# Kernel optimization log

Measured on AMD Instinct MI355X. Metric: run time of the kernel, lower is better.

Reference implementation:

```python
import jax, jax.numpy as jnp
import numpy as np


def setup_inputs() -> dict:
    key = jax.random.key(0)
    k1, k2, k3, k4 = jax.random.split(key, 4)
    B, S, D_IN, D_OUT = 4, 4096, 768, 128
    x = jax.random.normal(k1, (B, S, D_IN), dtype=jnp.float32)
    # torch Linear(d_in, d_out) weight is [d_out, d_in]; we store transposed [d_in, d_out]
    scale = 1.0 / np.sqrt(D_IN)
    Wq = jax.random.normal(k2, (D_IN, D_OUT), dtype=jnp.float32) * scale
    Wk = jax.random.normal(k3, (D_IN, D_OUT), dtype=jnp.float32) * scale
    Wv = jax.random.normal(k4, (D_IN, D_OUT), dtype=jnp.float32) * scale
    return {"x": x, "Wq": Wq, "Wk": Wk, "Wv": Wv}


def reference(x, Wq, Wk, Wv):
    # x: [B, S, d_in]; Wq/Wk/Wv: [d_in, d_out]
    B, S, _ = x.shape
    q = jnp.einsum('bsd,de->bse', x, Wq)
    k = jnp.einsum('bsd,de->bse', x, Wk)
    v = jnp.einsum('bsd,de->bse', x, Wv)
    d_out = k.shape[-1]
    scores = jnp.einsum('bqe,bke->bqk', q, k)  # [B, S, S]
    causal = jnp.tril(jnp.ones((S, S), dtype=bool))  # True where attention allowed
    scores = jnp.where(causal[None], scores, -jnp.inf)
    attn = jax.nn.softmax(scores / jnp.sqrt(jnp.float32(d_out)), axis=-1)
    # dropout prob is 0.0 -> identity
    return jnp.einsum('bqk,bke->bqe', attn, v)
```

## Files before the change

### kernel.cpp

```cpp
#include <hip/hip_runtime.h>
#include <stdint.h>

typedef unsigned short u16;
typedef uint32_t u32;
typedef __bf16 bf16;
typedef bf16 bf16x8 __attribute__((ext_vector_type(8)));
typedef bf16 bf16x4 __attribute__((ext_vector_type(4)));
typedef short s16x4 __attribute__((ext_vector_type(4)));
typedef float f32x4 __attribute__((ext_vector_type(4)));
typedef uint32_t u32x4 __attribute__((ext_vector_type(4)));

#define S_LEN 4096
#define D_IN 768
#define D_OUT 128
#define NB 4
#define M_TOTAL (NB * S_LEN)
#define NPROP 115

__device__ const unsigned char SPLITS_T[16] = {1,2,3,4,4,5,6,7,8,8,9,10,11,12,12,13};
__device__ const unsigned char OFF_T[16]    = {0,1,3,6,10,14,19,25,32,40,48,57,67,78,90,102};
__device__ const unsigned char TILE_OF[NPROP] = {
    0, 1,1, 2,2,2, 3,3,3,3, 4,4,4,4, 5,5,5,5,5, 6,6,6,6,6,6, 7,7,7,7,7,7,7,
    8,8,8,8,8,8,8,8, 9,9,9,9,9,9,9,9, 10,10,10,10,10,10,10,10,10,
    11,11,11,11,11,11,11,11,11,11, 12,12,12,12,12,12,12,12,12,12,12,
    13,13,13,13,13,13,13,13,13,13,13,13, 14,14,14,14,14,14,14,14,14,14,14,14,
    15,15,15,15,15,15,15,15,15,15,15,15,15};

static __device__ __forceinline__ u16 f2bf(float f) {
    union { float f; uint32_t u; } c; c.f = f;
    return (u16)((c.u + 0x7FFFu + ((c.u >> 16) & 1u)) >> 16);
}
static __device__ __forceinline__ float bf2f_lo(uint32_t w) { return __uint_as_float(w << 16); }
static __device__ __forceinline__ float bf2f_hi(uint32_t w) { return __uint_as_float(w & 0xFFFF0000u); }

static __device__ __forceinline__ bf16x8 ld8(const u16* p) {
    union { u32x4 v; bf16x8 b; } c;
    c.v = *reinterpret_cast<const u32x4*>(p);
    return c.b;
}

static __device__ __forceinline__ f32x4 mfma16(bf16x8 a, bf16x8 b, f32x4 c) {
    return __builtin_amdgcn_mfma_f32_16x16x32_bf16(a, b, c, 0, 0, 0);
}

static __device__ __forceinline__ f32x4 mfma16k16(uint2 a, uint2 b, f32x4 c) {
#if defined(__HIP_DEVICE_COMPILE__)
#if __has_builtin(__builtin_amdgcn_mfma_f32_16x16x16_bf16)
    union { uint2 u; bf16x4 v; } ca, cb; ca.u = a; cb.u = b;
    return __builtin_amdgcn_mfma_f32_16x16x16_bf16(ca.v, cb.v, c, 0, 0, 0);
#else
    union { uint2 u; s16x4 v; } ca, cb; ca.u = a; cb.u = b;
    return __builtin_amdgcn_mfma_f32_16x16x16bf16_1k(ca.v, cb.v, c, 0, 0, 0);
#endif
#else
    (void)a; (void)b;
    return c;
#endif
}

static __device__ __forceinline__ void gload16(const void* g, void* l) {
    __builtin_amdgcn_global_load_lds((const __attribute__((address_space(1))) uint32_t*)g,
                                     (__attribute__((address_space(3))) uint32_t*)l, 16, 0, 0);
}

static __device__ __forceinline__ float bpermf(int addr, float v) {
    return __int_as_float(__builtin_amdgcn_ds_bpermute(addr, __float_as_int(v)));
}
static __device__ __forceinline__ u32 pk2(float a, float b) {
    return __builtin_amdgcn_perm(__float_as_uint(b), __float_as_uint(a), 0x07060302u);
}

__global__ __launch_bounds__(256) void wt_kernel(const float* __restrict__ Wq, const float* __restrict__ Wk,
                                                 const float* __restrict__ Wv, u16* __restrict__ Wt) {
    __shared__ u16 tl[128][40];
    const int w = blockIdx.x / 24;
    const int kc = (blockIdx.x % 24) * 32;
    const float* W = (w == 0) ? Wq : (w == 1) ? Wk : Wv;
#pragma unroll
    for (int p = 0; p < 4; ++p) {
        int kr = p * 8 + (threadIdx.x >> 5);
        int nc = (threadIdx.x & 31) * 4;
        float4 v = *reinterpret_cast<const float4*>(W + (size_t)(kc + kr) * D_OUT + nc);
        tl[nc + 0][kr] = f2bf(v.x); tl[nc + 1][kr] = f2bf(v.y);
        tl[nc + 2][kr] = f2bf(v.z); tl[nc + 3][kr] = f2bf(v.w);
    }
    __syncthreads();
    const int n = threadIdx.x >> 1, kh = (threadIdx.x & 1) * 16;
    u32x4* dst = reinterpret_cast<u32x4*>(Wt + (size_t)w * D_OUT * D_IN + (size_t)n * D_IN + kc + kh);
    const u32x4* src = reinterpret_cast<const u32x4*>(&tl[n][kh]);
    dst[0] = src[0];
    dst[1] = src[1];
}

__global__ __launch_bounds__(256) void qkv_kernel(const float* __restrict__ x, const u16* __restrict__ Wt,
                                                  u16* __restrict__ Qb, u16* __restrict__ Kb,
                                                  u16* __restrict__ Vt) {
    __shared__ __align__(16) u16 wslab[2][192 * 32];
    __shared__ __align__(16) float xslab[2][64 * 32];
    const int wave = threadIdx.x >> 6, lane = threadIdx.x & 63;
    const int r = lane & 15, g = lane >> 4;
    const int m0 = blockIdx.x * 64;
    const int h = blockIdx.y;

    f32x4 acc[3][4];
#pragma unroll
    for (int y = 0; y < 3; ++y)
#pragma unroll
        for (int f = 0; f < 4; ++f) acc[y][f] = f32x4{0.f, 0.f, 0.f, 0.f};

    auto stageW = [&](int bb, int kk) {
#pragma unroll
        for (int i = 0; i < 3; ++i) {
            int c = i * 4 + wave;
            int rr = c * 16 + (lane >> 2);
            int gr = (rr >> 6) * 128 + h * 64 + (rr & 63);
            const u16* src = Wt + (size_t)gr * D_IN + kk * 32 + (((lane & 3) ^ (rr & 3)) * 8);
            gload16(src, &wslab[bb][c * 512]);
        }
    };
    auto stageX = [&](int bb, int kk) {
#pragma unroll
        for (int i = 0; i < 2; ++i) {
            int c = i * 4 + wave;
            int row = c * 8 + (lane >> 3);
            const float* src = x + (size_t)(m0 + row) * D_IN + kk * 32 + (((lane & 7) ^ (row & 7)) * 4);
            gload16(src, &xslab[bb][c * 256]);
        }
    };

    stageW(0, 0);
    stageX(0, 0);
    int buf = 0;
    const int arow = wave * 16 + r;
    for (int kk = 0; kk < 24; ++kk) {
        int kn = (kk + 1 < 24) ? kk + 1 : 0;
        stageX(buf ^ 1, kn);
        stageW(buf ^ 1, kn);
        asm volatile("s_waitcnt vmcnt(5)" ::: "memory");
        __builtin_amdgcn_sched_barrier(0);
        __builtin_amdgcn_s_barrier();
        f32x4 xa0 = *reinterpret_cast<const f32x4*>(&xslab[buf][arow * 32 + (((2 * g) ^ (arow & 7)) * 4)]);
        f32x4 xa1 = *reinterpret_cast<const f32x4*>(&xslab[buf][arow * 32 + (((2 * g + 1) ^ (arow & 7)) * 4)]);
        union { u16 u[8]; bf16x8 bv; } af;
#pragma unroll
        for (int t = 0; t < 4; ++t) { af.u[t] = f2bf(xa0[t]); af.u[4 + t] = f2bf(xa1[t]); }
#pragma unroll
        for (int y = 0; y < 3; ++y)
#pragma unroll
            for (int f = 0; f < 4; ++f) {
                int rr = y * 64 + f * 16 + r;
                bf16x8 wf = ld8(&wslab[buf][rr * 32 + ((g ^ (r & 3)) * 8)]);
                acc[y][f] = mfma16(af.bv, wf, acc[y][f]);
            }
        __builtin_amdgcn_s_barrier();
        buf ^= 1;
    }
    asm volatile("s_waitcnt vmcnt(0)" ::: "memory");

    const float QSC = 0.1275174366f;
#pragma unroll
    for (int f = 0; f < 4; ++f)
#pragma unroll
        for (int i = 0; i < 4; ++i) {
            int mrow = m0 + wave * 16 + 4 * g + i;
            int col = h * 64 + f * 16 + r;
            Qb[(size_t)mrow * D_OUT + col] = f2bf(acc[0][f][i] * QSC);
            Kb[(size_t)mrow * D_OUT + col] = f2bf(acc[1][f][i]);
            Vt[((size_t)((mrow >> 12) * D_OUT + col)) * S_LEN + (mrow & 4095)] = f2bf(acc[2][f][i]);
        }
}

__global__ __launch_bounds__(512, 2) void attn_kernel(const u16* __restrict__ Qb, const u16* __restrict__ Kb,
                                                      const u16* __restrict__ Vt, u16* __restrict__ Po,
                                                      float* __restrict__ Pml, float* __restrict__ out,
                                                      int mode) {
    __shared__ __align__(16) u16 kbuf[2][64 * 128];
    __shared__ __align__(16) u16 vbuf[2][128 * 64];

    const int wave = threadIdx.x >> 6, lane = threadIdx.x & 63;
    const int r = lane & 15, g = lane >> 4;
    const int n = (int)blockIdx.x;
    int b, t, s, sp;
    if (mode) {
        b = n / NPROP;
        const int idx = n - b * NPROP;
        t = TILE_OF[idx];
        s = idx - OFF_T[t];
        sp = SPLITS_T[t];
    } else {
        b = n >> 4; t = n & 15; s = 0; sp = 1;
    }
    const int nj = 4 * t + 4;
    const int qw0 = t * 256 + wave * 32;

    const u16* Kp = Kb + (size_t)b * S_LEN * D_OUT;
    const u16* Vp = Vt + (size_t)b * D_OUT * S_LEN;

    bf16x8 qf[2][4];
#pragma unroll
    for (int rb = 0; rb < 2; ++rb)
#pragma unroll
        for (int kk = 0; kk < 4; ++kk)
            qf[rb][kk] = ld8(Qb + ((size_t)(b * S_LEN + qw0 + rb * 16 + r)) * D_OUT + kk * 32 + 8 * g);

    f32x4 o[2][8];
    float l_[2];
#pragma unroll
    for (int rb = 0; rb < 2; ++rb) {
#pragma unroll
        for (int f = 0; f < 8; ++f) o[rb][f] = f32x4{0.f, 0.f, 0.f, 0.f};
        l_[rb] = 0.f;
    }

    const int lx16 = (lane ^ 16) * 4, lx32 = (lane ^ 32) * 4;

    auto stageK = [&](int bb, int k0) {
#pragma unroll
        for (int i = 0; i < 2; ++i) {
            int c = i * 8 + wave;
            int row = c * 4 + (lane >> 4);
            const u16* src = Kp + (size_t)(k0 + row) * D_OUT + (((lane & 15) ^ (row & 7)) * 8);
            gload16(src, &kbuf[bb][c * 512]);
        }
    };
    auto stageV = [&](int bb, int k0) {
#pragma unroll
        for (int i = 0; i < 2; ++i) {
            int c = i * 8 + wave;
            int row = c * 8 + (lane >> 3);
            const u16* src = Vp + (size_t)row * S_LEN + k0 + (((lane & 7) ^ (row & 7)) * 8);
            gload16(src, &vbuf[bb][c * 512]);
        }
    };

    stageK(0, s * 64);
    stageV(0, s * 64);
    int buf = 0;
    for (int j = s; j < nj; j += sp) {
        const int k0 = j * 64;
        asm volatile("s_waitcnt vmcnt(0)" ::: "memory");
        __builtin_amdgcn_sched_barrier(0);
        __builtin_amdgcn_s_barrier();
        const int j2 = j + sp;
        if (j2 < nj) {
            stageK(buf ^ 1, j2 * 64);
            stageV(buf ^ 1, j2 * 64);
        }

        f32x4 sv[2][4];
#pragma unroll
        for (int rb = 0; rb < 2; ++rb)
#pragma unroll
            for (int f = 0; f < 4; ++f) sv[rb][f] = f32x4{0.f, 0.f, 0.f, 0.f};
        __builtin_amdgcn_s_setprio(1);
#pragma unroll
        for (int kk = 0; kk < 4; ++kk)
#pragma unroll
            for (int f = 0; f < 4; ++f) {
                bf16x8 kf = ld8(&kbuf[buf][(f * 16 + r) * 128 + (((kk * 4 + g) ^ (r & 7)) * 8)]);
                sv[0][f] = mfma16(kf, qf[0][kk], sv[0][f]);
                sv[1][f] = mfma16(kf, qf[1][kk], sv[1][f]);
            }
        __builtin_amdgcn_s_setprio(0);

        uint2 pb[2][4];
#pragma unroll
        for (int rb = 0; rb < 2; ++rb) {
            const int qrb = qw0 + rb * 16;
            const int q = qrb + r;
            if (k0 + 63 > qrb) {
#pragma unroll
                for (int f = 0; f < 4; ++f)
#pragma unroll
                    for (int i = 0; i < 4; ++i)
                        if (k0 + 16 * f + 4 * g + i > q) sv[rb][f][i] = -1e30f;
            }
            float r0 = 0.f;
#pragma unroll
            for (int f = 0; f < 4; ++f)
#pragma unroll
                for (int i = 0; i < 4; ++i) {
                    float p = __builtin_amdgcn_exp2f(sv[rb][f][i]);
                    sv[rb][f][i] = p;
                    r0 += p;
                }
            l_[rb] += r0;
#pragma unroll
            for (int kb = 0; kb < 4; ++kb) {
                pb[rb][kb].x = pk2(sv[rb][kb][0], sv[rb][kb][1]);
                pb[rb][kb].y = pk2(sv[rb][kb][2], sv[rb][kb][3]);
            }
        }

        __builtin_amdgcn_s_setprio(1);
#pragma unroll
        for (int kb = 0; kb < 4; ++kb) {
            const int vs = ((2 * kb + (g >> 1)) ^ (r & 7)) * 8 + 4 * (g & 1);
#pragma unroll
            for (int f = 0; f < 8; ++f) {
                uint2 vf = *reinterpret_cast<const uint2*>(&vbuf[buf][(f * 16 + r) * 64 + vs]);
                o[0][f] = mfma16k16(vf, pb[0][kb], o[0][f]);
                o[1][f] = mfma16k16(vf, pb[1][kb], o[1][f]);
            }
        }
        __builtin_amdgcn_s_setprio(0);
        buf ^= 1;
    }
    asm volatile("s_waitcnt vmcnt(0)" ::: "memory");

    l_[0] += bpermf(lx16, l_[0]);
    l_[1] += bpermf(lx16, l_[1]);
    l_[0] += bpermf(lx32, l_[0]);
    l_[1] += bpermf(lx32, l_[1]);

    if (!mode) {
#pragma unroll
        for (int rb = 0; rb < 2; ++rb) {
            float inv = 1.0f / l_[rb];
            float* orow = out + ((size_t)(b * S_LEN + qw0 + rb * 16 + r)) * D_OUT;
#pragma unroll
            for (int f = 0; f < 8; ++f) {
                float4 v;
                v.x = o[rb][f][0] * inv; v.y = o[rb][f][1] * inv;
                v.z = o[rb][f][2] * inv; v.w = o[rb][f][3] * inv;
                *reinterpret_cast<float4*>(orow + 16 * f + 4 * g) = v;
            }
        }
    } else {
        u16* po = Po + (size_t)n * (256 * 128);
        float* pml = Pml + (size_t)n * 512;
#pragma unroll
        for (int rb = 0; rb < 2; ++rb) {
            u16* chunk0 = po + (size_t)((wave * 2 + rb) * 8) * 256 + lane * 4;
#pragma unroll
            for (int f = 0; f < 8; ++f) {
                u32 w0 = (u32)f2bf(o[rb][f][0]) | ((u32)f2bf(o[rb][f][1]) << 16);
                u32 w1 = (u32)f2bf(o[rb][f][2]) | ((u32)f2bf(o[rb][f][3]) << 16);
                uint2 ww; ww.x = w0; ww.y = w1;
                *reinterpret_cast<uint2*>(chunk0 + f * 256) = ww;
            }
            if (g == 0) {
                const int row = wave * 32 + rb * 16 + r;
                pml[row * 2 + 0] = 0.f;
                pml[row * 2 + 1] = l_[rb];
            }
        }
    }
}

__global__ __launch_bounds__(256) void merge_kernel(const u16* __restrict__ Po, const float* __restrict__ Pml,
                                                    float* __restrict__ out) {
    const int gr = blockIdx.x * 16 + (threadIdx.x >> 4);
    const int c0 = (threadIdx.x & 15) * 8;
    const int b = gr >> 12, rr = gr & 4095;
    const int t = rr >> 8, row = rr & 255;
    const int ns = SPLITS_T[t];
    const size_t pbase = (size_t)b * NPROP + OFF_T[t];

    const int wv = row >> 5, rbm = (row >> 4) & 1, r_ = row & 15;
    const int fm = c0 >> 4, g0 = (c0 >> 2) & 3;
    const size_t coff = (size_t)((wv * 2 + rbm) * 8 + fm) * 256;

    float L = 0.f;
    for (int s = 0; s < ns; ++s) L += Pml[(pbase + s) * 512 + row * 2 + 1];
    const float inv = 1.0f / L;

    float acc[8];
#pragma unroll
    for (int k = 0; k < 8; ++k) acc[k] = 0.f;
    for (int s = 0; s < ns; ++s) {
        const u16* chunk = Po + (pbase + s) * (256 * 128) + coff;
        uint2 pv0 = *reinterpret_cast<const uint2*>(chunk + (g0 * 16 + r_) * 4);
        uint2 pv1 = *reinterpret_cast<const uint2*>(chunk + ((g0 + 1) * 16 + r_) * 4);
        acc[0] += bf2f_lo(pv0.x); acc[1] += bf2f_hi(pv0.x);
        acc[2] += bf2f_lo(pv0.y); acc[3] += bf2f_hi(pv0.y);
        acc[4] += bf2f_lo(pv1.x); acc[5] += bf2f_hi(pv1.x);
        acc[6] += bf2f_lo(pv1.y); acc[7] += bf2f_hi(pv1.y);
    }
    float* op = out + (size_t)gr * D_OUT + c0;
    float4 v0, v1;
    v0.x = acc[0] * inv; v0.y = acc[1] * inv; v0.z = acc[2] * inv; v0.w = acc[3] * inv;
    v1.x = acc[4] * inv; v1.y = acc[5] * inv; v1.z = acc[6] * inv; v1.w = acc[7] * inv;
    *reinterpret_cast<float4*>(op) = v0;
    *reinterpret_cast<float4*>(op + 4) = v1;
}

extern "C" void kernel_launch(void* const* d_in, const int* in_sizes, int n_in,
                              void* d_out, int out_size, void* d_ws, size_t ws_size,
                              hipStream_t stream) {
    const float* x  = (const float*)d_in[0];
    const float* Wq = (const float*)d_in[1];
    const float* Wk = (const float*)d_in[2];
    const float* Wv = (const float*)d_in[3];
    float* out = (float*)d_out;

    u16* Qb = (u16*)d_ws;
    u16* Kb = Qb + (size_t)M_TOTAL * D_OUT;
    u16* Vt = Kb + (size_t)M_TOTAL * D_OUT;
    u16* Wt = Vt + (size_t)M_TOTAL * D_OUT;

    const unsigned long long base = (3ULL * M_TOTAL * D_OUT + 3ULL * D_OUT * D_IN) * 2ULL;
    const unsigned long long perP = 256ULL * 128 * 2 + 512ULL * 4;
    const int nblk = NPROP * NB;
    const int mode = (ws_size >= base + (unsigned long long)nblk * perP) ? 1 : 0;

    u16* Po = Wt + (size_t)3 * D_OUT * D_IN;
    float* Pml = (float*)(Po + (size_t)nblk * (256 * 128));

    wt_kernel<<<72, 256, 0, stream>>>(Wq, Wk, Wv, Wt);
    qkv_kernel<<<dim3(256, 2), 256, 0, stream>>>(x, Wt, Qb, Kb, Vt);
    attn_kernel<<<mode ? nblk : 16 * NB, 512, 0, stream>>>(Qb, Kb, Vt, Po, Pml, out, mode);
    if (mode)
        merge_kernel<<<M_TOTAL / 16, 256, 0, stream>>>(Po, Pml, out);
}
```

Before: 89.76 us.

## Double K-step in QKV projection, convert x to bf16 in registers before LDS staging

The QKV projection kernel now processes 64-wide K chunks (12 iterations instead of 24). It loads x through registers, packs it to bf16 and writes it into a swizzled bf16 LDS slab, where before fp32 was copied straight to LDS and converted after every read. Fewer iterations mean fewer barriers, and LDS traffic for x is halved. In exchange, the register-path x load replaces the async direct-to-LDS copy, waits are now full vmcnt(0), and the second barrier per iteration is dropped, which shifts how load latency overlaps with MFMA work.

```diff
diff --git a/kernel.cpp b/kernel.cpp
--- a/kernel.cpp
+++ b/kernel.cpp
@@ -95,8 +95,8 @@
 __global__ __launch_bounds__(256) void qkv_kernel(const float* __restrict__ x, const u16* __restrict__ Wt,
                                                   u16* __restrict__ Qb, u16* __restrict__ Kb,
                                                   u16* __restrict__ Vt) {
-    __shared__ __align__(16) u16 wslab[2][192 * 32];
-    __shared__ __align__(16) float xslab[2][64 * 32];
+    __shared__ __align__(16) u16 wslab[2][192 * 64];
+    __shared__ __align__(16) u16 xslab[2][64 * 64];
     const int wave = threadIdx.x >> 6, lane = threadIdx.x & 63;
     const int r = lane & 15, g = lane >> 4;
     const int m0 = blockIdx.x * 64;
@@ -110,49 +110,60 @@
 
     auto stageW = [&](int bb, int kk) {
 #pragma unroll
-        for (int i = 0; i < 3; ++i) {
+        for (int i = 0; i < 6; ++i) {
             int c = i * 4 + wave;
-            int rr = c * 16 + (lane >> 2);
+            int rr = c * 8 + (lane >> 3);
             int gr = (rr >> 6) * 128 + h * 64 + (rr & 63);
-            const u16* src = Wt + (size_t)gr * D_IN + kk * 32 + (((lane & 3) ^ (rr & 3)) * 8);
+            int slot = (lane & 7) ^ (rr & 7);
+            const u16* src = Wt + (size_t)gr * D_IN + kk * 64 + slot * 8;
             gload16(src, &wslab[bb][c * 512]);
         }
     };
-    auto stageX = [&](int bb, int kk) {
-#pragma unroll
-        for (int i = 0; i < 2; ++i) {
-            int c = i * 4 + wave;
-            int row = c * 8 + (lane >> 3);
-            const float* src = x + (size_t)(m0 + row) * D_IN + kk * 32 + (((lane & 7) ^ (row & 7)) * 4);
-            gload16(src, &xslab[bb][c * 256]);
-        }
+    auto loadX = [&](int kk, float4* v) {
+        const float* src = x + (size_t)(m0 + (threadIdx.x >> 2)) * D_IN + kk * 64 + (threadIdx.x & 3) * 16;
+        v[0] = *reinterpret_cast<const float4*>(src);
+        v[1] = *reinterpret_cast<const float4*>(src + 4);
+        v[2] = *reinterpret_cast<const float4*>(src + 8);
+        v[3] = *reinterpret_cast<const float4*>(src + 12);
     };
-
+    auto writeX = [&](int bb, const float4* v) {
+        const int row = threadIdx.x >> 2, w2 = (threadIdx.x & 3) * 2;
+        u32x4 p0, p1;
+        p0[0] = pk2(v[0].x, v[0].y); p0[1] = pk2(v[0].z, v[0].w);
+        p0[2] = pk2(v[1].x, v[1].y); p0[3] = pk2(v[1].z, v[1].w);
+        p1[0] = pk2(v[2].x, v[2].y); p1[1] = pk2(v[2].z, v[2].w);
+        p1[2] = pk2(v[3].x, v[3].y); p1[3] = pk2(v[3].z, v[3].w);
+        *reinterpret_cast<u32x4*>(&xslab[bb][row * 64 + ((w2 ^ (row & 7)) * 8)]) = p0;
+        *reinterpret_cast<u32x4*>(&xslab[bb][row * 64 + (((w2 + 1) ^ (row & 7)) * 8)]) = p1;
+    };
+
+    float4 xv[4];
     stageW(0, 0);
-    stageX(0, 0);
+    loadX(0, xv);
     int buf = 0;
     const int arow = wave * 16 + r;
-    for (int kk = 0; kk < 24; ++kk) {
-        int kn = (kk + 1 < 24) ? kk + 1 : 0;
-        stageX(buf ^ 1, kn);
-        stageW(buf ^ 1, kn);
-        asm volatile("s_waitcnt vmcnt(5)" ::: "memory");
+    for (int kk = 0; kk < 12; ++kk) {
+        writeX(buf, xv);
+        asm volatile("s_waitcnt lgkmcnt(0)" ::: "memory");
+        asm volatile("s_waitcnt vmcnt(0)" ::: "memory");
         __builtin_amdgcn_sched_barrier(0);
         __builtin_amdgcn_s_barrier();
-        f32x4 xa0 = *reinterpret_cast<const f32x4*>(&xslab[buf][arow * 32 + (((2 * g) ^ (arow & 7)) * 4)]);
-        f32x4 xa1 = *reinterpret_cast<const f32x4*>(&xslab[buf][arow * 32 + (((2 * g + 1) ^ (arow & 7)) * 4)]);
-        union { u16 u[8]; bf16x8 bv; } af;
-#pragma unroll
-        for (int t = 0; t < 4; ++t) { af.u[t] = f2bf(xa0[t]); af.u[4 + t] = f2bf(xa1[t]); }
-#pragma unroll
-        for (int y = 0; y < 3; ++y)
-#pragma unroll
-            for (int f = 0; f < 4; ++f) {
-                int rr = y * 64 + f * 16 + r;
-                bf16x8 wf = ld8(&wslab[buf][rr * 32 + ((g ^ (r & 3)) * 8)]);
-                acc[y][f] = mfma16(af.bv, wf, acc[y][f]);
-            }
-        __builtin_amdgcn_s_barrier();
+        if (kk + 1 < 12) {
+            stageW(buf ^ 1, kk + 1);
+            loadX(kk + 1, xv);
+        }
+#pragma unroll
+        for (int kk2 = 0; kk2 < 2; ++kk2) {
+            bf16x8 xa = ld8(&xslab[buf][arow * 64 + (((kk2 * 4 + g) ^ (arow & 7)) * 8)]);
+#pragma unroll
+            for (int y = 0; y < 3; ++y)
+#pragma unroll
+                for (int f = 0; f < 4; ++f) {
+                    int rr = y * 64 + f * 16 + r;
+                    bf16x8 wf = ld8(&wslab[buf][rr * 64 + (((kk2 * 4 + g) ^ (rr & 7)) * 8)]);
+                    acc[y][f] = mfma16(xa, wf, acc[y][f]);
+                }
+        }
         buf ^= 1;
     }
     asm volatile("s_waitcnt vmcnt(0)" ::: "memory");
```

Result: no change. 89.31 us (-0.5%).
